# Kernel tuning notes

Hardware: AMD Instinct MI355X
Metric: run time of the kernel (lower is better)

## Reference

```python
import jax, jax.numpy as jnp
import numpy as np

E = 64          # num_routed experts
K = 6           # top-k activated experts per token
CAP = 1536
BAL = 0.01      # balance_factor


def _gelu(x):
    # torch nn.GELU default is exact (erf) gelu
    return jax.nn.gelu(x, approximate=False)


def setup_inputs() -> dict:
    key = jax.random.key(0)
    ks = jax.random.split(key, 8)
    B, N, D, H = 2, 2048, 768, 1536
    x = jax.random.normal(ks[0], (B, N, D), jnp.float32)
    gate_w = jax.random.normal(ks[1], (E, D), jnp.float32) * (D ** -0.5)
    sh1_w = jax.random.normal(ks[2], (H, D), jnp.float32) * (D ** -0.5)
    sh1_b = jnp.zeros((H,), jnp.float32)
    sh2_w = jax.random.normal(ks[3], (D, H), jnp.float32) * (H ** -0.5)
    sh2_b = jnp.zeros((D,), jnp.float32)
    e1_w = jax.random.normal(ks[4], (E, H, D), jnp.float32) * (D ** -0.5)
    e1_b = jnp.zeros((E, H), jnp.float32)
    e2_w = jax.random.normal(ks[5], (E, D, H), jnp.float32) * (H ** -0.5)
    e2_b = jnp.zeros((E, D), jnp.float32)
    return {"x": x, "gate_w": gate_w, "sh1_w": sh1_w, "sh1_b": sh1_b,
            "sh2_w": sh2_w, "sh2_b": sh2_b, "e1_w": e1_w, "e1_b": e1_b,
            "e2_w": e2_w, "e2_b": e2_b}


def reference(x, gate_w, sh1_w, sh1_b, sh2_w, sh2_b, e1_w, e1_b, e2_w, e2_b):
    B, N, D = x.shape
    T = B * N
    # shared expert (dense MLP, drop=0)
    sh = _gelu(jnp.einsum('bnd,hd->bnh', x, sh1_w) + sh1_b)
    shared_out = jnp.einsum('bnh,dh->bnd', sh, sh2_w) + sh2_b
    # gating
    gate_scores = jax.nn.softmax(jnp.einsum('bnd,ed->bne', x, gate_w), axis=-1)
    top_s, top_i = jax.lax.top_k(gate_scores, K)          # (B,N,K)
    flat_x = x.reshape(T, D)
    pair_tok = jnp.repeat(jnp.arange(T), K)               # (T*K,)
    pair_exp = top_i.reshape(-1)
    pair_sc = top_s.reshape(-1)
    # sort pairs by expert (stable, matching torch argsort(stable=True))
    order = jnp.argsort(pair_exp, stable=True)
    s_tok = pair_tok[order]
    s_exp = pair_exp[order]
    s_sc = pair_sc[order]
    s_x = flat_x[s_tok]                                   # (T*K, D)
    counts = jnp.bincount(s_exp, length=E)                # (E,)
    offs = jnp.concatenate([jnp.zeros((1,), counts.dtype), jnp.cumsum(counts)])
    pos = jnp.arange(T * K) - offs[s_exp]                 # slot within expert
    # pad into (E, CAP, D); out-of-capacity updates are dropped (never hit at this scale)
    padded_x = jnp.zeros((E, CAP, D), x.dtype).at[s_exp, pos].set(s_x)
    padded_sc = jnp.zeros((E, CAP), x.dtype).at[s_exp, pos].set(s_sc)
    # grouped expert GEMMs
    h = _gelu(jnp.einsum('ecd,ehd->ech', padded_x, e1_w) + e1_b[:, None, :])
    out = jnp.einsum('ech,edh->ecd', h, e2_w) + e2_b[:, None, :]
    out = out * padded_sc[..., None]
    # un-pad and scatter-add combine back to tokens
    valid = out[s_exp, pos]                               # (T*K, D)
    routed_out = jnp.zeros((T, D), x.dtype).at[s_tok].add(valid).reshape(B, N, D)
    # balance loss terms
    expert_freq = counts.astype(x.dtype) / (T * K)
    expert_prob = gate_scores.reshape(T, E).mean(axis=0)
    balance_loss = BAL * jnp.sum(expert_freq * expert_prob)
    return shared_out + routed_out, balance_loss, expert_freq, expert_prob
```

## Files before the change

### kernel.cpp

```cpp
#include <hip/hip_runtime.h>
#include <stdint.h>

#define T_TOKENS 4096
#define D_DIM 768
#define H_DIM 1536
#define NEXP 64
#define TOPK 6
#define CAP 1536
#define MAXTILES 288
#define MAXROWS (MAXTILES*128)

typedef __bf16 bf16x8 __attribute__((ext_vector_type(8)));
typedef float f32x4 __attribute__((ext_vector_type(4)));

__device__ __forceinline__ ushort f2bf(float f) {
    union { float f; uint32_t u; } v; v.f = f;
    uint32_t r = v.u + 0x7FFFu + ((v.u >> 16) & 1u);
    return (ushort)(r >> 16);
}

__global__ __launch_bounds__(256)
void gate_kernel(const float* __restrict__ x, const float* __restrict__ gate_w,
                 int* __restrict__ cnt, float* __restrict__ prob_sum,
                 int* __restrict__ tok_of, float* __restrict__ sc_of)
{
    __shared__ float xs[16 * 768];
    __shared__ float sred[4][64];
    const int tid = threadIdx.x;
    const int t0 = blockIdx.x * 16;
    const float4* xg = (const float4*)(x + (size_t)t0 * 768);
    float4* xs4w = (float4*)xs;
    #pragma unroll
    for (int c = 0; c < 12; ++c) xs4w[c * 256 + tid] = xg[c * 256 + tid];
    __syncthreads();
    const int lane = tid & 63;
    const int wv = tid >> 6;
    float dots[4] = {0.f, 0.f, 0.f, 0.f};
    const float4* w4 = (const float4*)(gate_w + (size_t)lane * 768);
    const float4* xs4 = (const float4*)xs;
    for (int d = 0; d < 192; ++d) {
        float4 w = w4[d];
        #pragma unroll
        for (int tt = 0; tt < 4; ++tt) {
            float4 xv = xs4[(wv * 4 + tt) * 192 + d];
            dots[tt] += w.x * xv.x + w.y * xv.y + w.z * xv.z + w.w * xv.w;
        }
    }
    float psum_local = 0.f;
    for (int tt = 0; tt < 4; ++tt) {
        const int t = t0 + wv * 4 + tt;
        float z = dots[tt];
        float m = z;
        #pragma unroll
        for (int off = 32; off; off >>= 1) m = fmaxf(m, __shfl_xor(m, off));
        float ex = expf(z - m);
        float s = ex;
        #pragma unroll
        for (int off = 32; off; off >>= 1) s += __shfl_xor(s, off);
        float p = ex / s;
        psum_local += p;
        float pv = p;
        for (int k = 0; k < TOPK; ++k) {
            float v = pv; int widx = lane;
            #pragma unroll
            for (int off = 32; off; off >>= 1) {
                float ov = __shfl_xor(v, off);
                int oi = __shfl_xor(widx, off);
                if (ov > v || (ov == v && oi < widx)) { v = ov; widx = oi; }
            }
            if (lane == widx) {
                int pos = atomicAdd(&cnt[lane], 1);
                if (pos < CAP) { tok_of[lane * CAP + pos] = t; sc_of[lane * CAP + pos] = p; }
                pv = -1.0f;
            }
        }
    }
    sred[wv][lane] = psum_local;
    __syncthreads();
    if (wv == 0) {
        float tot = sred[0][lane] + sred[1][lane] + sred[2][lane] + sred[3][lane];
        atomicAdd(&prob_sum[lane], tot);
    }
}

__global__ void stats_kernel(const int* __restrict__ cnt, const float* __restrict__ prob_sum,
                             int* __restrict__ off, int* __restrict__ d_total_tiles,
                             int* __restrict__ tile_expert, float* __restrict__ out_tail)
{
    __shared__ int soff[66];
    __shared__ float sfp[64];
    const int tid = threadIdx.x;
    if (tid == 0) {
        int o = 0;
        for (int e = 0; e < NEXP; ++e) {
            soff[e] = o;
            int c = cnt[e]; if (c > CAP) c = CAP;
            o += ((c + 127) >> 7) << 7;
        }
        soff[64] = o;
        soff[65] = o + T_TOKENS;
        *d_total_tiles = (o + T_TOKENS) >> 7;
    }
    __syncthreads();
    if (tid < 66) off[tid] = soff[tid];
    const int total = soff[65] >> 7;
    for (int tile = tid; tile < MAXTILES; tile += blockDim.x) {
        if (tile < total) {
            int e = 0;
            for (int q = 1; q < 65; ++q) if (soff[q] <= tile * 128) e = q;
            tile_expert[tile] = e;
        }
    }
    if (tid < 64) {
        float f  = (float)cnt[tid] * (1.0f / 24576.0f);
        float pr = prob_sum[tid] * (1.0f / 4096.0f);
        out_tail[1 + tid] = f;
        out_tail[1 + 64 + tid] = pr;
        sfp[tid] = f * pr;
    }
    __syncthreads();
    if (tid == 0) {
        float l = 0.f;
        for (int e = 0; e < NEXP; ++e) l += sfp[e];
        out_tail[0] = 0.01f * l;
    }
}

__global__ __launch_bounds__(192)
void gather_kernel(const float* __restrict__ x,
                   const int* __restrict__ off, const int* __restrict__ cnt,
                   const int* __restrict__ tile_expert, const int* __restrict__ d_total_tiles,
                   const int* __restrict__ tok_of, const float* __restrict__ sc_of,
                   ushort* __restrict__ Xg, int* __restrict__ row_tok, float* __restrict__ row_score)
{
    const int row = blockIdx.x;
    if (row >= (*d_total_tiles) * 128) return;
    const int e = tile_expert[row >> 7];
    const int r = row - off[e];
    int t = 0; float sc = 0.f; bool real = false;
    if (e == NEXP) { t = r; sc = 1.0f; real = true; }
    else {
        int c = cnt[e]; if (c > CAP) c = CAP;
        if (r < c) { t = tok_of[e * CAP + r]; sc = sc_of[e * CAP + r]; real = true; }
    }
    const int tid = threadIdx.x;
    ushort4* dst = (ushort4*)(Xg + (size_t)row * 768);
    if (real) {
        float4 v = ((const float4*)(x + (size_t)t * 768))[tid];
        ushort4 o; o.x = f2bf(v.x); o.y = f2bf(v.y); o.z = f2bf(v.z); o.w = f2bf(v.w);
        dst[tid] = o;
    } else {
        dst[tid] = make_ushort4(0, 0, 0, 0);
    }
    if (tid == 0) { row_tok[row] = t; row_score[row] = real ? sc : 0.0f; }
}

template<int KD, int ND, bool DOGELU>
__global__ __launch_bounds__(256, 2)
void gemm_kernel(const ushort* __restrict__ Abuf,
                 const float* __restrict__ Wexp, const float* __restrict__ Wsh,
                 const float* __restrict__ Bexp, const float* __restrict__ Bsh,
                 const int* __restrict__ d_total_tiles, const int* __restrict__ tile_expert,
                 ushort* __restrict__ Hout, float* __restrict__ Cout,
                 const int* __restrict__ row_tok, const float* __restrict__ row_score)
{
    const int mt = blockIdx.x;
    if (mt >= *d_total_tiles) return;
    const int e = tile_expert[mt];
    const float* W  = (e < NEXP) ? (Wexp + (size_t)e * ND * KD) : Wsh;
    const float* Bi = (e < NEXP) ? (Bexp + (size_t)e * ND) : Bsh;
    const int row0 = mt * 128;
    const int n0 = blockIdx.y * 128;

    __shared__ ushort sA[128][72];
    __shared__ ushort sB[128][72];

    const int tid = threadIdx.x;
    const int lane = tid & 63;
    const int wv = tid >> 6;
    const int wm = (wv >> 1) << 6;
    const int wn = (wv & 1) << 6;
    const int lm = lane & 15;
    const int lq = lane >> 4;

    f32x4 acc[4][4] = {};

    for (int ks = 0; ks < KD / 64; ++ks) {
        const int k0 = ks * 64;
        #pragma unroll
        for (int c = 0; c < 4; ++c) {
            int idx = c * 256 + tid;
            int r = idx >> 3;
            int c8 = (idx & 7) << 3;
            uint4 v = *(const uint4*)(Abuf + (size_t)(row0 + r) * KD + (k0 + c8));
            *(uint4*)&sA[r][c8] = v;
        }
        #pragma unroll
        for (int c = 0; c < 8; ++c) {
            int idx = c * 256 + tid;
            int r = idx >> 4;
            int c4 = (idx & 15) << 2;
            float4 wv4 = *(const float4*)(W + (size_t)(n0 + r) * KD + (k0 + c4));
            ushort4 h4;
            h4.x = f2bf(wv4.x); h4.y = f2bf(wv4.y); h4.z = f2bf(wv4.z); h4.w = f2bf(wv4.w);
            *(ushort4*)&sB[r][c4] = h4;
        }
        __syncthreads();
        #pragma unroll
        for (int kk = 0; kk < 2; ++kk) {
            bf16x8 af[4], bfr[4];
            #pragma unroll
            for (int i = 0; i < 4; ++i)
                af[i] = *(const bf16x8*)&sA[wm + i * 16 + lm][kk * 32 + lq * 8];
            #pragma unroll
            for (int j = 0; j < 4; ++j)
                bfr[j] = *(const bf16x8*)&sB[wn + j * 16 + lm][kk * 32 + lq * 8];
            #pragma unroll
            for (int i = 0; i < 4; ++i)
                #pragma unroll
                for (int j = 0; j < 4; ++j)
                    acc[i][j] = __builtin_amdgcn_mfma_f32_16x16x32_bf16(af[i], bfr[j], acc[i][j], 0, 0, 0);
        }
        __syncthreads();
    }

    if constexpr (DOGELU) {
        #pragma unroll
        for (int i = 0; i < 4; ++i) {
            int gm = row0 + wm + i * 16 + lq * 4;
            #pragma unroll
            for (int j = 0; j < 4; ++j) {
                int gn = n0 + wn + j * 16 + lm;
                float bb = Bi[gn];
                #pragma unroll
                for (int r = 0; r < 4; ++r) {
                    float v = acc[i][j][r] + bb;
                    v = 0.5f * v * (1.0f + erff(v * 0.70710678118654752f));
                    Hout[(size_t)(gm + r) * ND + gn] = f2bf(v);
                }
            }
        }
    } else {
        #pragma unroll
        for (int i = 0; i < 4; ++i) {
            int gmb = row0 + wm + i * 16 + lq * 4;
            #pragma unroll
            for (int r = 0; r < 4; ++r) {
                int gm = gmb + r;
                float sc = row_score[gm];
                if (sc != 0.0f) {
                    int t = row_tok[gm];
                    float* dst = Cout + (size_t)t * D_DIM;
                    #pragma unroll
                    for (int j = 0; j < 4; ++j) {
                        int gn = n0 + wn + j * 16 + lm;
                        float v = (acc[i][j][r] + Bi[gn]) * sc;
                        atomicAdd(dst + gn, v);
                    }
                }
            }
        }
    }
}

extern "C" void kernel_launch(void* const* d_in, const int* in_sizes, int n_in,
                              void* d_out, int out_size, void* d_ws, size_t ws_size,
                              hipStream_t stream)
{
    const float* x      = (const float*)d_in[0];
    const float* gate_w = (const float*)d_in[1];
    const float* sh1_w  = (const float*)d_in[2];
    const float* sh1_b  = (const float*)d_in[3];
    const float* sh2_w  = (const float*)d_in[4];
    const float* sh2_b  = (const float*)d_in[5];
    const float* e1_w   = (const float*)d_in[6];
    const float* e1_b   = (const float*)d_in[7];
    const float* e2_w   = (const float*)d_in[8];
    const float* e2_b   = (const float*)d_in[9];
    float* out = (float*)d_out;

    char* ws = (char*)d_ws;
    int*    cnt       = (int*)(ws + 0);
    float*  prob_sum  = (float*)(ws + 1024);
    int*    off       = (int*)(ws + 2048);
    int*    total_t   = (int*)(ws + 3072);
    int*    tile_exp  = (int*)(ws + 4096);
    int*    tok_of    = (int*)(ws + 8192);
    float*  sc_of     = (float*)(ws + 8192 + (size_t)64 * CAP * 4);
    int*    row_tok   = (int*)(ws + 8192 + (size_t)2 * 64 * CAP * 4);
    float*  row_score = (float*)(ws + 8192 + (size_t)2 * 64 * CAP * 4 + (size_t)MAXROWS * 4);
    ushort* Xg        = (ushort*)(ws + (size_t)2 * 1024 * 1024);
    ushort* Hbuf      = (ushort*)(ws + (size_t)2 * 1024 * 1024 + (size_t)MAXROWS * 768 * 2);

    hipMemsetAsync(ws, 0, 2048, stream);
    hipMemsetAsync(d_out, 0, (size_t)out_size * 4, stream);

    gate_kernel<<<T_TOKENS / 16, 256, 0, stream>>>(x, gate_w, cnt, prob_sum, tok_of, sc_of);
    stats_kernel<<<1, 256, 0, stream>>>(cnt, prob_sum, off, total_t, tile_exp, out + (size_t)T_TOKENS * D_DIM);
    gather_kernel<<<MAXROWS, 192, 0, stream>>>(x, off, cnt, tile_exp, total_t, tok_of, sc_of, Xg, row_tok, row_score);

    dim3 g1(MAXTILES, H_DIM / 128);
    gemm_kernel<D_DIM, H_DIM, true><<<g1, 256, 0, stream>>>(
        Xg, e1_w, sh1_w, e1_b, sh1_b, total_t, tile_exp, Hbuf, nullptr, nullptr, nullptr);

    dim3 g2(MAXTILES, D_DIM / 128);
    gemm_kernel<H_DIM, D_DIM, false><<<g2, 256, 0, stream>>>(
        Hbuf, e2_w, sh2_w, e2_b, sh2_b, total_t, tile_exp, nullptr, out, row_tok, row_score);
}
```

Measured before the change: 1.130 ms.

## Prefetch next K-tile into registers and interleave tile order in expert GEMM

Restructures the GEMM main loop so the next K-slice of activations and weights is loaded into registers while MFMAs run on the current shared-memory tile, overlapping global loads with compute. It also remaps block indices so consecutive blocks spread across the tile range, and raises the occupancy hint to three blocks per SM. Weight stores now use packed 16-byte writes. The prefetch registers increase register pressure, which can conflict with the higher occupancy target and cause spills.

```diff
diff --git a/kernel.cpp b/kernel.cpp
--- a/kernel.cpp
+++ b/kernel.cpp
@@ -17,6 +17,10 @@
     union { float f; uint32_t u; } v; v.f = f;
     uint32_t r = v.u + 0x7FFFu + ((v.u >> 16) & 1u);
     return (ushort)(r >> 16);
+}
+
+__device__ __forceinline__ uint32_t pkbf(float lo, float hi) {
+    return (uint32_t)f2bf(lo) | ((uint32_t)f2bf(hi) << 16);
 }
 
 __global__ __launch_bounds__(256)
@@ -156,7 +160,7 @@
 }
 
 template<int KD, int ND, bool DOGELU>
-__global__ __launch_bounds__(256, 2)
+__global__ __launch_bounds__(256, 3)
 void gemm_kernel(const ushort* __restrict__ Abuf,
                  const float* __restrict__ Wexp, const float* __restrict__ Wsh,
                  const float* __restrict__ Bexp, const float* __restrict__ Bsh,
@@ -164,7 +168,7 @@
                  ushort* __restrict__ Hout, float* __restrict__ Cout,
                  const int* __restrict__ row_tok, const float* __restrict__ row_score)
 {
-    const int mt = blockIdx.x;
+    const int mt = (blockIdx.x & 7) * (MAXTILES / 8) + (blockIdx.x >> 3);
     if (mt >= *d_total_tiles) return;
     const int e = tile_expert[mt];
     const float* W  = (e < NEXP) ? (Wexp + (size_t)e * ND * KD) : Wsh;
@@ -183,29 +187,45 @@
     const int lm = lane & 15;
     const int lq = lane >> 4;
 
+    const int rb = tid >> 3;
+    const int c8 = (tid & 7) << 3;
+
+    const ushort* Ap = Abuf + (size_t)(row0 + rb) * KD + c8;
+    const float*  Wp = W    + (size_t)(n0   + rb) * KD + c8;
+
     f32x4 acc[4][4] = {};
-
-    for (int ks = 0; ks < KD / 64; ++ks) {
-        const int k0 = ks * 64;
+    uint4  apf[4];
+    float4 wpf[8];
+
+    constexpr int NK = KD / 64;
+
+    #pragma unroll
+    for (int c = 0; c < 4; ++c) {
+        apf[c]       = *(const uint4*) (Ap + (size_t)c * 32 * KD);
+        wpf[2*c]     = *(const float4*)(Wp + (size_t)c * 32 * KD);
+        wpf[2*c + 1] = *(const float4*)(Wp + (size_t)c * 32 * KD + 4);
+    }
+
+    for (int ks = 0; ks < NK; ++ks) {
         #pragma unroll
         for (int c = 0; c < 4; ++c) {
-            int idx = c * 256 + tid;
-            int r = idx >> 3;
-            int c8 = (idx & 7) << 3;
-            uint4 v = *(const uint4*)(Abuf + (size_t)(row0 + r) * KD + (k0 + c8));
-            *(uint4*)&sA[r][c8] = v;
-        }
-        #pragma unroll
-        for (int c = 0; c < 8; ++c) {
-            int idx = c * 256 + tid;
-            int r = idx >> 4;
-            int c4 = (idx & 15) << 2;
-            float4 wv4 = *(const float4*)(W + (size_t)(n0 + r) * KD + (k0 + c4));
-            ushort4 h4;
-            h4.x = f2bf(wv4.x); h4.y = f2bf(wv4.y); h4.z = f2bf(wv4.z); h4.w = f2bf(wv4.w);
-            *(ushort4*)&sB[r][c4] = h4;
+            *(uint4*)&sA[rb + 32 * c][c8] = apf[c];
+            float4 wa = wpf[2*c], wb = wpf[2*c + 1];
+            uint4 u;
+            u.x = pkbf(wa.x, wa.y); u.y = pkbf(wa.z, wa.w);
+            u.z = pkbf(wb.x, wb.y); u.w = pkbf(wb.z, wb.w);
+            *(uint4*)&sB[rb + 32 * c][c8] = u;
         }
         __syncthreads();
+        if (ks + 1 < NK) {
+            const int k0 = (ks + 1) * 64;
+            #pragma unroll
+            for (int c = 0; c < 4; ++c) {
+                apf[c]       = *(const uint4*) (Ap + (size_t)c * 32 * KD + k0);
+                wpf[2*c]     = *(const float4*)(Wp + (size_t)c * 32 * KD + k0);
+                wpf[2*c + 1] = *(const float4*)(Wp + (size_t)c * 32 * KD + k0 + 4);
+            }
+        }
         #pragma unroll
         for (int kk = 0; kk < 2; ++kk) {
             bf16x8 af[4], bfr[4];
```

New measurement: 1.447 ms. +28.0%, slower.

## Fuse token gather into first GEMM and retile GEMMs to 512 threads

Applied to the files above, without the earlier changes.

Removes the separate gather kernel that materialized a bf16 copy of the routed token rows. The first GEMM now reads rows of x directly through a row-to-token map and converts them to bf16 while staging into shared memory, avoiding a write and re-read of the gathered buffer. Both GEMMs move to 512-thread blocks with a 32-wide K step and 64x32 per-wave tiles, and a blockIdx remap spreads tiles across expert groups. Halving the K chunk doubles the number of barrier pairs per tile, and the padded-row gather reads are uncoalesced.

```diff
diff --git a/kernel.cpp b/kernel.cpp
--- a/kernel.cpp
+++ b/kernel.cpp
@@ -126,45 +126,36 @@
     }
 }
 
-__global__ __launch_bounds__(192)
-void gather_kernel(const float* __restrict__ x,
-                   const int* __restrict__ off, const int* __restrict__ cnt,
+__global__ __launch_bounds__(256)
+void rowmap_kernel(const int* __restrict__ off, const int* __restrict__ cnt,
                    const int* __restrict__ tile_expert, const int* __restrict__ d_total_tiles,
                    const int* __restrict__ tok_of, const float* __restrict__ sc_of,
-                   ushort* __restrict__ Xg, int* __restrict__ row_tok, float* __restrict__ row_score)
-{
-    const int row = blockIdx.x;
+                   int* __restrict__ row_tok, float* __restrict__ row_score)
+{
+    const int row = blockIdx.x * 256 + threadIdx.x;
     if (row >= (*d_total_tiles) * 128) return;
     const int e = tile_expert[row >> 7];
     const int r = row - off[e];
-    int t = 0; float sc = 0.f; bool real = false;
-    if (e == NEXP) { t = r; sc = 1.0f; real = true; }
+    int t = -1; float sc = 0.f;
+    if (e == NEXP) { t = r; sc = 1.0f; }
     else {
         int c = cnt[e]; if (c > CAP) c = CAP;
-        if (r < c) { t = tok_of[e * CAP + r]; sc = sc_of[e * CAP + r]; real = true; }
-    }
-    const int tid = threadIdx.x;
-    ushort4* dst = (ushort4*)(Xg + (size_t)row * 768);
-    if (real) {
-        float4 v = ((const float4*)(x + (size_t)t * 768))[tid];
-        ushort4 o; o.x = f2bf(v.x); o.y = f2bf(v.y); o.z = f2bf(v.z); o.w = f2bf(v.w);
-        dst[tid] = o;
-    } else {
-        dst[tid] = make_ushort4(0, 0, 0, 0);
-    }
-    if (tid == 0) { row_tok[row] = t; row_score[row] = real ? sc : 0.0f; }
-}
-
-template<int KD, int ND, bool DOGELU>
-__global__ __launch_bounds__(256, 2)
-void gemm_kernel(const ushort* __restrict__ Abuf,
+        if (r < c) { t = tok_of[e * CAP + r]; sc = sc_of[e * CAP + r]; }
+    }
+    row_tok[row] = t;
+    row_score[row] = sc;
+}
+
+template<int KD, int ND, bool DOGELU, bool GATHERX>
+__global__ __launch_bounds__(512, 2)
+void gemm_kernel(const ushort* __restrict__ Abuf, const float* __restrict__ Xsrc,
                  const float* __restrict__ Wexp, const float* __restrict__ Wsh,
                  const float* __restrict__ Bexp, const float* __restrict__ Bsh,
                  const int* __restrict__ d_total_tiles, const int* __restrict__ tile_expert,
                  ushort* __restrict__ Hout, float* __restrict__ Cout,
                  const int* __restrict__ row_tok, const float* __restrict__ row_score)
 {
-    const int mt = blockIdx.x;
+    const int mt = (blockIdx.x & 7) * (MAXTILES / 8) + (blockIdx.x >> 3);
     if (mt >= *d_total_tiles) return;
     const int e = tile_expert[mt];
     const float* W  = (e < NEXP) ? (Wexp + (size_t)e * ND * KD) : Wsh;
@@ -172,55 +163,75 @@
     const int row0 = mt * 128;
     const int n0 = blockIdx.y * 128;
 
-    __shared__ ushort sA[128][72];
-    __shared__ ushort sB[128][72];
+    __shared__ ushort sA[128][40];
+    __shared__ ushort sB[128][40];
 
     const int tid = threadIdx.x;
     const int lane = tid & 63;
     const int wv = tid >> 6;
-    const int wm = (wv >> 1) << 6;
-    const int wn = (wv & 1) << 6;
+    const int wm = (wv >> 2) << 6;
+    const int wn = (wv & 3) << 5;
     const int lm = lane & 15;
     const int lq = lane >> 4;
 
-    f32x4 acc[4][4] = {};
-
-    for (int ks = 0; ks < KD / 64; ++ks) {
-        const int k0 = ks * 64;
-        #pragma unroll
-        for (int c = 0; c < 4; ++c) {
-            int idx = c * 256 + tid;
-            int r = idx >> 3;
-            int c8 = (idx & 7) << 3;
-            uint4 v = *(const uint4*)(Abuf + (size_t)(row0 + r) * KD + (k0 + c8));
-            *(uint4*)&sA[r][c8] = v;
-        }
-        #pragma unroll
-        for (int c = 0; c < 8; ++c) {
-            int idx = c * 256 + tid;
-            int r = idx >> 4;
-            int c4 = (idx & 15) << 2;
-            float4 wv4 = *(const float4*)(W + (size_t)(n0 + r) * KD + (k0 + c4));
-            ushort4 h4;
-            h4.x = f2bf(wv4.x); h4.y = f2bf(wv4.y); h4.z = f2bf(wv4.z); h4.w = f2bf(wv4.w);
-            *(ushort4*)&sB[r][c4] = h4;
+    const int rb = tid >> 3;
+    const int c4 = (tid & 7) << 2;
+
+    const float* Wp = W + (size_t)(n0 + rb) * KD + c4;
+
+    const float* xp[2];
+    const ushort* Ap = nullptr;
+    int ar = 0, ac8 = 0;
+    if constexpr (GATHERX) {
+        #pragma unroll
+        for (int c = 0; c < 2; ++c) {
+            int t = row_tok[row0 + rb + 64 * c];
+            xp[c] = (t >= 0) ? (Xsrc + (size_t)t * KD + c4) : nullptr;
+        }
+    } else {
+        ar = tid >> 2;
+        ac8 = (tid & 3) << 3;
+        Ap = Abuf + (size_t)(row0 + ar) * KD + ac8;
+    }
+
+    f32x4 acc[4][2] = {};
+    constexpr int NK = KD / 32;
+
+    for (int ks = 0; ks < NK; ++ks) {
+        const int k0 = ks * 32;
+        if constexpr (GATHERX) {
+            #pragma unroll
+            for (int c = 0; c < 2; ++c) {
+                float4 v = xp[c] ? *(const float4*)(xp[c] + k0)
+                                 : make_float4(0.f, 0.f, 0.f, 0.f);
+                ushort4 u;
+                u.x = f2bf(v.x); u.y = f2bf(v.y); u.z = f2bf(v.z); u.w = f2bf(v.w);
+                *(ushort4*)&sA[rb + 64 * c][c4] = u;
+            }
+        } else {
+            uint4 v = *(const uint4*)(Ap + k0);
+            *(uint4*)&sA[ar][ac8] = v;
+        }
+        #pragma unroll
+        for (int c = 0; c < 2; ++c) {
+            float4 v = *(const float4*)(Wp + (size_t)c * 64 * KD + k0);
+            ushort4 u;
+            u.x = f2bf(v.x); u.y = f2bf(v.y); u.z = f2bf(v.z); u.w = f2bf(v.w);
+            *(ushort4*)&sB[rb + 64 * c][c4] = u;
         }
         __syncthreads();
-        #pragma unroll
-        for (int kk = 0; kk < 2; ++kk) {
-            bf16x8 af[4], bfr[4];
-            #pragma unroll
-            for (int i = 0; i < 4; ++i)
-                af[i] = *(const bf16x8*)&sA[wm + i * 16 + lm][kk * 32 + lq * 8];
-            #pragma unroll
-            for (int j = 0; j < 4; ++j)
-                bfr[j] = *(const bf16x8*)&sB[wn + j * 16 + lm][kk * 32 + lq * 8];
-            #pragma unroll
-            for (int i = 0; i < 4; ++i)
-                #pragma unroll
-                for (int j = 0; j < 4; ++j)
-                    acc[i][j] = __builtin_amdgcn_mfma_f32_16x16x32_bf16(af[i], bfr[j], acc[i][j], 0, 0, 0);
-        }
+        bf16x8 af[4], bfr[2];
+        #pragma unroll
+        for (int i = 0; i < 4; ++i)
+            af[i] = *(const bf16x8*)&sA[wm + i * 16 + lm][lq * 8];
+        #pragma unroll
+        for (int j = 0; j < 2; ++j)
+            bfr[j] = *(const bf16x8*)&sB[wn + j * 16 + lm][lq * 8];
+        #pragma unroll
+        for (int i = 0; i < 4; ++i)
+            #pragma unroll
+            for (int j = 0; j < 2; ++j)
+                acc[i][j] = __builtin_amdgcn_mfma_f32_16x16x32_bf16(af[i], bfr[j], acc[i][j], 0, 0, 0);
         __syncthreads();
     }
 
@@ -229,7 +240,7 @@
         for (int i = 0; i < 4; ++i) {
             int gm = row0 + wm + i * 16 + lq * 4;
             #pragma unroll
-            for (int j = 0; j < 4; ++j) {
+            for (int j = 0; j < 2; ++j) {
                 int gn = n0 + wn + j * 16 + lm;
                 float bb = Bi[gn];
                 #pragma unroll
@@ -252,7 +263,7 @@
                     int t = row_tok[gm];
                     float* dst = Cout + (size_t)t * D_DIM;
                     #pragma unroll
-                    for (int j = 0; j < 4; ++j) {
+                    for (int j = 0; j < 2; ++j) {
                         int gn = n0 + wn + j * 16 + lm;
                         float v = (acc[i][j][r] + Bi[gn]) * sc;
                         atomicAdd(dst + gn, v);
@@ -289,21 +300,20 @@
     float*  sc_of     = (float*)(ws + 8192 + (size_t)64 * CAP * 4);
     int*    row_tok   = (int*)(ws + 8192 + (size_t)2 * 64 * CAP * 4);
     float*  row_score = (float*)(ws + 8192 + (size_t)2 * 64 * CAP * 4 + (size_t)MAXROWS * 4);
-    ushort* Xg        = (ushort*)(ws + (size_t)2 * 1024 * 1024);
-    ushort* Hbuf      = (ushort*)(ws + (size_t)2 * 1024 * 1024 + (size_t)MAXROWS * 768 * 2);
+    ushort* Hbuf      = (ushort*)(ws + (size_t)2 * 1024 * 1024);
 
     hipMemsetAsync(ws, 0, 2048, stream);
     hipMemsetAsync(d_out, 0, (size_t)out_size * 4, stream);
 
     gate_kernel<<<T_TOKENS / 16, 256, 0, stream>>>(x, gate_w, cnt, prob_sum, tok_of, sc_of);
     stats_kernel<<<1, 256, 0, stream>>>(cnt, prob_sum, off, total_t, tile_exp, out + (size_t)T_TOKENS * D_DIM);
-    gather_kernel<<<MAXROWS, 192, 0, stream>>>(x, off, cnt, tile_exp, total_t, tok_of, sc_of, Xg, row_tok, row_score);
+    rowmap_kernel<<<MAXROWS / 256, 256, 0, stream>>>(off, cnt, tile_exp, total_t, tok_of, sc_of, row_tok, row_score);
 
     dim3 g1(MAXTILES, H_DIM / 128);
-    gemm_kernel<D_DIM, H_DIM, true><<<g1, 256, 0, stream>>>(
-        Xg, e1_w, sh1_w, e1_b, sh1_b, total_t, tile_exp, Hbuf, nullptr, nullptr, nullptr);
+    gemm_kernel<D_DIM, H_DIM, true, true><<<g1, 512, 0, stream>>>(
+        nullptr, x, e1_w, sh1_w, e1_b, sh1_b, total_t, tile_exp, Hbuf, nullptr, row_tok, row_score);
 
     dim3 g2(MAXTILES, D_DIM / 128);
-    gemm_kernel<H_DIM, D_DIM, false><<<g2, 256, 0, stream>>>(
-        Hbuf, e2_w, sh2_w, e2_b, sh2_b, total_t, tile_exp, nullptr, out, row_tok, row_score);
-}
+    gemm_kernel<H_DIM, D_DIM, false, false><<<g2, 512, 0, stream>>>(
+        Hbuf, nullptr, e2_w, sh2_w, e2_b, sh2_b, total_t, tile_exp, nullptr, out, row_tok, row_score);
+}
```

Result: no change. 1.129 ms (-0.1%).
